# Kernel tuning notes

Hardware: AMD Instinct MI355X
Metric: run time of the kernel (lower is better)

The kernel has to match this reference:

```python
import jax, jax.numpy as jnp
import numpy as np
from math import sqrt

RELATIVE_CUTOFF = 128
VALUE_DIM = 64


def _skew(m):
    # m: (b, h, S, 2S-1) -> (b, h, S, S), out[i, j] = m[i, j - i + S - 1]
    b, h, S, _ = m.shape
    m = jnp.pad(m, ((0, 0), (0, 0), (0, 0), (0, 1)))          # (b,h,S,2S)
    m = m.reshape(b, h, 2 * S * S)
    m = jnp.pad(m, ((0, 0), (0, 0), (0, S - 1)))
    m = m.reshape(b, h, S + 1, 2 * S - 1)
    return m[:, :, :S, S - 1:]


def setup_inputs() -> dict:
    key = jax.random.key(0)
    ks = jax.random.split(key, 5)
    B, S, E, H, Dk, Dv = 2, 2048, 512, 8, 64, 64
    return {
        "xs": jax.random.normal(ks[0], (B, S, E), dtype=jnp.float32),
        "w_q": jax.random.normal(ks[1], (H, E, Dk), dtype=jnp.float32) * (1.0 / sqrt(E)),
        "w_k": jax.random.normal(ks[2], (H, E, Dk), dtype=jnp.float32) * (1.0 / sqrt(E)),
        "w_v": jax.random.normal(ks[3], (H, E, Dv), dtype=jnp.float32) * (1.0 / sqrt(E)),
        "w_o": jnp.ones((H,), dtype=jnp.float32),
        "a_k": jax.random.normal(ks[4], (2 * RELATIVE_CUTOFF + 1, Dk), dtype=jnp.float32) * 0.1,
    }


def reference(xs, w_q, w_k, w_v, w_o, a_k):
    S = xs.shape[1]
    queries = jnp.einsum("bse,heq->bhsq", xs, w_q)
    keys = jnp.einsum("bse,hek->bhsk", xs, w_k)
    values = jnp.einsum("bse,hev->bhsv", xs, w_v)

    # relative positional embeddings: pos in [-S+1, S-1], clamped to cutoff
    pos = jnp.clip(jnp.arange(-S + 1, S), -RELATIVE_CUTOFF, RELATIVE_CUTOFF) + RELATIVE_CUTOFF
    rel = a_k[pos]                                             # (2S-1, Dk)

    q_k = jnp.einsum("bhiq,bhjq->bhij", queries, keys)
    q_rel = _skew(jnp.einsum("bhiq,rq->bhir", queries, rel))   # (b,h,S,S)

    e = (q_k + q_rel) / sqrt(VALUE_DIM)
    alphas = jax.nn.softmax(e, axis=3)
    z = jnp.einsum("bhij,bhjv->bhiv", alphas, values)
    return jnp.einsum("bhsv,h->bsv", z, w_o)
```

## Files before the change

### kernel.cpp

```cpp
#include <hip/hip_runtime.h>
#include <hip/hip_bf16.h>

#define S_LEN 2048
#define E_DIM 512
#define D_DIM 64
#define H_NUM 8
#define B_NUM 2
#define BH_NUM 16
#define NQA 257
#define QAE_W 512
#define KSPLIT 2
#define NP 8
#define QTILE 256
#define BNDW 176

typedef _Float16 half8 __attribute__((ext_vector_type(8)));
typedef float f32x16 __attribute__((ext_vector_type(16)));
typedef unsigned int uint2v __attribute__((ext_vector_type(2)));
typedef unsigned int uint4v __attribute__((ext_vector_type(4)));

static __device__ __forceinline__ f32x16 MFMA(half8 a, half8 b, f32x16 c) {
    return __builtin_amdgcn_mfma_f32_32x32x16_f16(a, b, c, 0, 0, 0);
}
static __device__ __forceinline__ f32x16 ZERO16() {
    f32x16 z;
    #pragma unroll
    for (int i = 0; i < 16; ++i) z[i] = 0.f;
    return z;
}
static __device__ __forceinline__ unsigned int PKRTZ(float a, float b) {
    return __builtin_bit_cast(unsigned int, __builtin_amdgcn_cvt_pkrtz(a, b));
}

__global__ __launch_bounds__(256) void cast_x_kernel(
    const float* __restrict__ xs, _Float16* __restrict__ Xh)
{
    const int idx = (blockIdx.x * 256 + threadIdx.x) * 8;
    float4 a = *(const float4*)&xs[idx];
    float4 b = *(const float4*)&xs[idx + 4];
    half8 o;
    o[0] = (_Float16)a.x; o[1] = (_Float16)a.y; o[2] = (_Float16)a.z; o[3] = (_Float16)a.w;
    o[4] = (_Float16)b.x; o[5] = (_Float16)b.y; o[6] = (_Float16)b.z; o[7] = (_Float16)b.w;
    *(half8*)&Xh[idx] = o;
}

__global__ __launch_bounds__(256) void cast_wak_kernel(
    const float* __restrict__ w_q, const float* __restrict__ w_k,
    const float* __restrict__ w_v, const float* __restrict__ w_o,
    const float* __restrict__ a_k,
    _Float16* __restrict__ Wht, _Float16* __restrict__ akh)
{
    __shared__ float T[64][68];
    const int type = blockIdx.z;
    const int t = threadIdx.x;
    if (type == 3) {
        const int bn = blockIdx.y * 8 + blockIdx.x;
        if (bn >= 9) return;
        const int idx = (bn * 256 + t) * 8;
        if (idx < NQA * 64) {
            float4 a = *(const float4*)&a_k[idx];
            float4 b = *(const float4*)&a_k[idx + 4];
            half8 o;
            o[0] = (_Float16)a.x; o[1] = (_Float16)a.y; o[2] = (_Float16)a.z; o[3] = (_Float16)a.w;
            o[4] = (_Float16)b.x; o[5] = (_Float16)b.y; o[6] = (_Float16)b.z; o[7] = (_Float16)b.w;
            *(half8*)&akh[idx] = o;
        }
        return;
    }
    const int kt = blockIdx.x, h = blockIdx.y;
    const float* W = (type == 0) ? w_q : (type == 1) ? w_k : w_v;
    const float scale = (type == 0) ? 0.125f : (type == 2 ? w_o[h] : 1.0f);
    const int kr = t >> 2, nseg = (t & 3) * 16;
    #pragma unroll
    for (int i = 0; i < 4; ++i)
        *(float4*)&T[kr][nseg + 4 * i] =
            *(const float4*)&W[((size_t)h * 512 + kt * 64 + kr) * 64 + nseg + 4 * i];
    __syncthreads();
    const int nr = t >> 2, kseg = (t & 3) * 16;
    _Float16* dst = Wht + ((size_t)(type * 8 + h) * 64 + nr) * 512 + kt * 64 + kseg;
    #pragma unroll
    for (int i = 0; i < 2; ++i) {
        half8 o;
        #pragma unroll
        for (int j = 0; j < 8; ++j) o[j] = (_Float16)(T[kseg + 8 * i + j][nr] * scale);
        *(half8*)&dst[8 * i] = o;
    }
}

__global__ __launch_bounds__(256) void proj_mfma_kernel(
    const _Float16* __restrict__ Xh, const _Float16* __restrict__ Wht,
    const _Float16* __restrict__ akh,
    _Float16* __restrict__ Qh, _Float16* __restrict__ Kh,
    _Float16* __restrict__ Vt, _Float16* __restrict__ QAe)
{
    __shared__ __align__(16) _Float16 raw[30208];
    _Float16 (*Xlds)[128][72] = (_Float16(*)[128][72])raw;
    _Float16 (*Wlds)[64][72]  = (_Float16(*)[64][72])(raw + 18432);
    _Float16* ob  = raw;
    _Float16 (*ak)[72] = (_Float16(*)[72])(raw + 9216);
    _Float16* SLo = raw + 29952;
    _Float16* SHi = raw + 30080;

    const int mt = blockIdx.x, bh = blockIdx.y, type = blockIdx.z;
    const int b = bh >> 3, h = bh & 7;
    const int m0 = mt * 128;
    const int t = threadIdx.x, wid = t >> 6, lane = t & 63;
    const int lq = lane & 31, lh = lane >> 5;

    const _Float16* W = Wht + (size_t)(type * 8 + h) * 64 * 512;
    const _Float16* X = Xh + ((size_t)b * S_LEN + m0) * 512;

    const int xrow = t >> 1, xseg = (t & 1) * 32;
    const int wrow = t >> 2, wseg = (t & 3) * 16;

    #pragma unroll
    for (int i = 0; i < 4; ++i)
        *(half8*)&Xlds[0][xrow][xseg + 8 * i] =
            *(const half8*)&X[(size_t)xrow * 512 + xseg + 8 * i];
    #pragma unroll
    for (int i = 0; i < 2; ++i)
        *(half8*)&Wlds[0][wrow][wseg + 8 * i] =
            *(const half8*)&W[(size_t)wrow * 512 + wseg + 8 * i];
    __syncthreads();

    f32x16 acc[2];
    acc[0] = ZERO16(); acc[1] = ZERO16();
    int cur = 0;
    for (int c = 0; c < 8; ++c) {
        half8 xst[4], wst[2];
        if (c < 7) {
            const int k0 = (c + 1) * 64;
            #pragma unroll
            for (int i = 0; i < 4; ++i)
                xst[i] = *(const half8*)&X[(size_t)xrow * 512 + k0 + xseg + 8 * i];
            #pragma unroll
            for (int i = 0; i < 2; ++i)
                wst[i] = *(const half8*)&W[(size_t)wrow * 512 + k0 + wseg + 8 * i];
        }
        #pragma unroll
        for (int kc = 0; kc < 4; ++kc) {
            half8 a  = *(const half8*)&Xlds[cur][wid * 32 + lq][kc * 16 + lh * 8];
            half8 b0 = *(const half8*)&Wlds[cur][lq][kc * 16 + lh * 8];
            half8 b1 = *(const half8*)&Wlds[cur][32 + lq][kc * 16 + lh * 8];
            acc[0] = MFMA(a, b0, acc[0]);
            acc[1] = MFMA(a, b1, acc[1]);
        }
        if (c < 7) {
            #pragma unroll
            for (int i = 0; i < 4; ++i)
                *(half8*)&Xlds[cur ^ 1][xrow][xseg + 8 * i] = xst[i];
            #pragma unroll
            for (int i = 0; i < 2; ++i)
                *(half8*)&Wlds[cur ^ 1][wrow][wseg + 8 * i] = wst[i];
        }
        __syncthreads();
        cur ^= 1;
    }

    #pragma unroll
    for (int n = 0; n < 2; ++n)
        #pragma unroll
        for (int r = 0; r < 16; ++r) {
            int row = wid * 32 + (r & 3) + ((r >> 2) << 3) + (lh << 2);
            ob[row * 72 + n * 32 + lq] = (_Float16)acc[n][r];
        }
    __syncthreads();

    if (type == 2) {
        const int v = t >> 2, sseg = (t & 3) * 32;
        _Float16* dst = Vt + ((size_t)bh * 64 + v) * S_LEN + m0 + sseg;
        #pragma unroll
        for (int i = 0; i < 4; ++i) {
            half8 o;
            #pragma unroll
            for (int j = 0; j < 8; ++j) o[j] = ob[(sseg + 8 * i + j) * 72 + v];
            *(half8*)&dst[8 * i] = o;
        }
        return;
    }

    {
        _Float16* P = (type == 0) ? Qh : Kh;
        const int row = t >> 1, seg = (t & 1) * 32;
        _Float16* dst = P + ((size_t)bh * S_LEN + m0 + row) * 64 + seg;
        #pragma unroll
        for (int i = 0; i < 4; ++i)
            *(half8*)&dst[8 * i] = *(const half8*)&ob[row * 72 + seg + 8 * i];
    }
    if (type != 0) return;

    for (int r = t; r < 288; r += 256) {
        if (r < NQA) {
            #pragma unroll
            for (int i = 0; i < 8; ++i)
                *(half8*)&ak[r][8 * i] = *(const half8*)&akh[(size_t)r * 64 + 8 * i];
        } else {
            half8 z = {};
            #pragma unroll
            for (int i = 0; i < 8; ++i) *(half8*)&ak[r][8 * i] = z;
        }
    }
    __syncthreads();

    half8 qfr[4];
    #pragma unroll
    for (int kc = 0; kc < 4; ++kc)
        qfr[kc] = *(const half8*)&ob[(wid * 32 + lq) * 72 + kc * 16 + lh * 8];

    for (int nsub = 0; nsub < 9; ++nsub) {
        f32x16 qa = ZERO16();
        #pragma unroll
        for (int kc = 0; kc < 4; ++kc) {
            half8 bf = *(const half8*)&ak[nsub * 32 + lq][kc * 16 + lh * 8];
            qa = MFMA(qfr[kc], bf, qa);
        }
        const int col = nsub * 32 + lq;
        if (col < NQA) {
            #pragma unroll
            for (int r = 0; r < 16; ++r) {
                const int row = m0 + wid * 32 + (r & 3) + ((r >> 2) << 3) + (lh << 2);
                const _Float16 v = (_Float16)qa[r];
                QAe[((size_t)bh * S_LEN + row) * QAE_W + col + 128] = v;
                if (col == 0)   SLo[row - m0] = v;
                if (col == 256) SHi[row - m0] = v;
            }
        }
    }
    __syncthreads();

    const int prow = t >> 1, pseg = (t & 1) * 64;
    const _Float16 lo = SLo[prow], hi = SHi[prow];
    half8 vlo, vhi;
    #pragma unroll
    for (int j = 0; j < 8; ++j) { vlo[j] = lo; vhi[j] = hi; }
    _Float16* pb = QAe + ((size_t)bh * S_LEN + m0 + prow) * QAE_W;
    #pragma unroll
    for (int i = 0; i < 8; ++i) {
        *(half8*)&pb[pseg + 8 * i] = vlo;
        *(half8*)&pb[384 + pseg + 8 * i] = vhi;
    }
}

__global__ __launch_bounds__(512) void attn_kernel(
    const _Float16* __restrict__ Qh, const _Float16* __restrict__ Kh,
    const _Float16* __restrict__ Vt, const _Float16* __restrict__ QAe,
    _Float16* __restrict__ Po, float2* __restrict__ Ml)
{
    __shared__ __align__(16) char smraw[36864];
    _Float16 (*Klds)[64][72] = (_Float16(*)[64][72])smraw;
    _Float16 (*Vlds)[64][72] = (_Float16(*)[64][72])(smraw + 18432);
    _Float16* Obuf = (_Float16*)smraw;
    __shared__ __align__(16) _Float16 Bnd[8][32][BNDW];

    const int p0 = blockIdx.x;
    const int nb = (p0 & 7) * 32 + (p0 >> 3);
    const int bh = nb >> 4;
    const int rem = nb & 15;
    const int qt = rem & 7, ks = rem >> 3;
    const int i0 = qt * QTILE;
    const int kv0 = ks * 128;

    const int t = threadIdx.x, wid = t >> 6, lane = t & 63;
    const int lq = lane & 31, lh = lane >> 5;
    const int i0w = i0 + wid * 32;
    const int qg = i0w + lq;

    half8 qf[4];
    #pragma unroll
    for (int kc = 0; kc < 4; ++kc)
        qf[kc] = *(const half8*)&Qh[((size_t)bh * S_LEN + qg) * 64 + kc * 16 + lh * 8];

    const _Float16* qaeRow = QAe + ((size_t)bh * S_LEN + qg) * QAE_W;
    const float qa_lo = (float)qaeRow[128];
    const float qa_hi = (float)qaeRow[384];
    const _Float16* BndSrc = QAe + ((size_t)bh * S_LEN + i0w) * QAE_W;

    float rm = -1e30f, rl = 0.f;
    f32x16 acco[2];
    acco[0] = ZERO16(); acco[1] = ZERO16();

    const int srow = t >> 3, sseg = (t & 7) * 8;
    const _Float16* Kbase = Kh + (size_t)bh * S_LEN * 64;
    const _Float16* Vbase = Vt + ((size_t)bh * 64 + srow) * S_LEN;

    const int brow = lane >> 1;
    const int bhalf = (lane & 1) * 88;

    half8 kA, kB, vA, vB, breg[11];
    {
        const int js = kv0;
        *(half8*)&Klds[0][srow][sseg] = *(const half8*)&Kbase[(size_t)(js + srow) * 64 + sseg];
        *(half8*)&Klds[1][srow][sseg] = *(const half8*)&Kbase[(size_t)(js + 64 + srow) * 64 + sseg];
        *(half8*)&Vlds[0][srow][sseg] = *(const half8*)&Vbase[js + sseg];
        *(half8*)&Vlds[1][srow][sseg] = *(const half8*)&Vbase[js + 64 + sseg];
        const int j1 = 256 + kv0;
        kA = *(const half8*)&Kbase[(size_t)(j1 + srow) * 64 + sseg];
        kB = *(const half8*)&Kbase[(size_t)(j1 + 64 + srow) * 64 + sseg];
        vA = *(const half8*)&Vbase[j1 + sseg];
        vB = *(const half8*)&Vbase[j1 + 64 + sseg];
    }
    bool bA_n, bB_n; int cw0_n = 0;
    {
        const int d = kv0 - i0w;
        bA_n = (d > -191) && (d < 159);
        bB_n = (d > -255) && (d < 95);
        if (bA_n || bB_n) {
            const int dFB = bA_n ? d : d + 64;
            cw0_n = (dFB + 225) & ~7;
            cw0_n = cw0_n > 336 ? 336 : cw0_n;
            #pragma unroll
            for (int i = 0; i < 11; ++i)
                breg[i] = *(const half8*)&BndSrc[(size_t)brow * QAE_W + cw0_n + bhalf + i * 8];
        }
    }
    __syncthreads();

    for (int p = 0; p < NP; ++p) {
        const int diff = p * 256 + kv0 - i0w;
        const bool bA = bA_n, bB = bB_n;
        const int cw0 = cw0_n;

        if (bA || bB) {
            #pragma unroll
            for (int i = 0; i < 11; ++i)
                *(half8*)&Bnd[wid][brow][bhalf + i * 8] = breg[i];
        }

        f32x16 accs[4];
        accs[0] = ZERO16(); accs[1] = ZERO16(); accs[2] = ZERO16(); accs[3] = ZERO16();
        __builtin_amdgcn_s_setprio(1);
        #pragma unroll
        for (int kc = 0; kc < 4; ++kc) {
            half8 a0 = *(const half8*)&Klds[0][lq][kc * 16 + lh * 8];
            half8 a1 = *(const half8*)&Klds[0][32 + lq][kc * 16 + lh * 8];
            half8 b0 = *(const half8*)&Klds[1][lq][kc * 16 + lh * 8];
            half8 b1 = *(const half8*)&Klds[1][32 + lq][kc * 16 + lh * 8];
            accs[0] = MFMA(a0, qf[kc], accs[0]);
            accs[1] = MFMA(a1, qf[kc], accs[1]);
            accs[2] = MFMA(b0, qf[kc], accs[2]);
            accs[3] = MFMA(b1, qf[kc], accs[3]);
        }
        __builtin_amdgcn_s_setprio(0);

        float bunif = 0.f;
        if (diff >= 159) {
            bunif = qa_hi;
        } else if (diff <= -255) {
            bunif = qa_lo;
        } else {
            asm volatile("s_waitcnt lgkmcnt(0)" ::: "memory");
            __builtin_amdgcn_sched_barrier(0);
            const int pbA = diff + 256 - cw0 - lq;
            const int pbB = pbA + 64;
            if (bA) {
                #pragma unroll
                for (int m = 0; m < 2; ++m)
                    #pragma unroll
                    for (int r = 0; r < 16; ++r) {
                        const int keyoff = m * 32 + (r & 3) + ((r >> 2) << 3) + (lh << 2);
                        accs[m][r] += (float)Bnd[wid][lq][pbA + keyoff];
                    }
            } else {
                #pragma unroll
                for (int m = 0; m < 2; ++m)
                    #pragma unroll
                    for (int r = 0; r < 16; ++r) accs[m][r] += qa_lo;
            }
            if (bB) {
                #pragma unroll
                for (int m = 0; m < 2; ++m)
                    #pragma unroll
                    for (int r = 0; r < 16; ++r) {
                        const int keyoff = m * 32 + (r & 3) + ((r >> 2) << 3) + (lh << 2);
                        accs[2 + m][r] += (float)Bnd[wid][lq][pbB + keyoff];
                    }
            } else {
                #pragma unroll
                for (int m = 0; m < 2; ++m)
                    #pragma unroll
                    for (int r = 0; r < 16; ++r) accs[2 + m][r] += qa_hi;
            }
        }

        float t8[8];
        #pragma unroll
        for (int i = 0; i < 8; ++i)
            t8[i] = fmaxf(fmaxf(accs[0][i], accs[0][i + 8]),
                          fmaxf(accs[1][i], accs[1][i + 8]));
        #pragma unroll
        for (int i = 0; i < 8; ++i)
            t8[i] = fmaxf(t8[i], fmaxf(fmaxf(accs[2][i], accs[2][i + 8]),
                                       fmaxf(accs[3][i], accs[3][i + 8])));
        float tmax = fmaxf(fmaxf(fmaxf(t8[0], t8[1]), fmaxf(t8[2], t8[3])),
                           fmaxf(fmaxf(t8[4], t8[5]), fmaxf(t8[6], t8[7])));
        tmax = fmaxf(tmax, __shfl_xor(tmax, 32));
        const float mnew = fmaxf(rm, tmax + bunif);
        const bool resc = __any(mnew > rm);
        const float corr = __expf(rm - mnew);
        const float shift = mnew - bunif;
        rm = mnew;

        #pragma unroll
        for (int s = 0; s < 4; ++s)
            #pragma unroll
            for (int r = 0; r < 16; ++r)
                accs[s][r] = __expf(accs[s][r] - shift);

        float s8[8];
        #pragma unroll
        for (int i = 0; i < 8; ++i)
            s8[i] = ((accs[0][i] + accs[0][i + 8]) + (accs[1][i] + accs[1][i + 8]))
                  + ((accs[2][i] + accs[2][i + 8]) + (accs[3][i] + accs[3][i + 8]));
        float psum = ((s8[0] + s8[1]) + (s8[2] + s8[3])) +
                     ((s8[4] + s8[5]) + (s8[6] + s8[7]));
        psum += __shfl_xor(psum, 32);

        if (resc) {
            rl = rl * corr + psum;
            #pragma unroll
            for (int n = 0; n < 2; ++n)
                #pragma unroll
                for (int r = 0; r < 16; ++r) acco[n][r] *= corr;
        } else {
            rl += psum;
        }

        half8 pfA[4], pfB[4];
        #pragma unroll
        for (int kc = 0; kc < 4; ++kc) {
            {
                const int m = kc >> 1, rb = (kc & 1) * 8;
                unsigned int a01 = PKRTZ(accs[m][rb + 0], accs[m][rb + 1]);
                unsigned int a45 = PKRTZ(accs[m][rb + 4], accs[m][rb + 5]);
                unsigned int a23 = PKRTZ(accs[m][rb + 2], accs[m][rb + 3]);
                unsigned int a67 = PKRTZ(accs[m][rb + 6], accs[m][rb + 7]);
                uint2v r02 = __builtin_amdgcn_permlane32_swap(a01, a45, false, false);
                uint2v r13 = __builtin_amdgcn_permlane32_swap(a23, a67, false, false);
                uint4v wv;
                wv[0] = r02[0]; wv[1] = r13[0]; wv[2] = r02[1]; wv[3] = r13[1];
                pfA[kc] = __builtin_bit_cast(half8, wv);
            }
            {
                const int m = 2 + (kc >> 1), rb = (kc & 1) * 8;
                unsigned int a01 = PKRTZ(accs[m][rb + 0], accs[m][rb + 1]);
                unsigned int a45 = PKRTZ(accs[m][rb + 4], accs[m][rb + 5]);
                unsigned int a23 = PKRTZ(accs[m][rb + 2], accs[m][rb + 3]);
                unsigned int a67 = PKRTZ(accs[m][rb + 6], accs[m][rb + 7]);
                uint2v r02 = __builtin_amdgcn_permlane32_swap(a01, a45, false, false);
                uint2v r13 = __builtin_amdgcn_permlane32_swap(a23, a67, false, false);
                uint4v wv;
                wv[0] = r02[0]; wv[1] = r13[0]; wv[2] = r02[1]; wv[3] = r13[1];
                pfB[kc] = __builtin_bit_cast(half8, wv);
            }
        }

        __builtin_amdgcn_s_setprio(1);
        #pragma unroll
        for (int kc = 0; kc < 4; ++kc) {
            half8 v0 = *(const half8*)&Vlds[0][lq][kc * 16 + lh * 8];
            half8 v1 = *(const half8*)&Vlds[0][32 + lq][kc * 16 + lh * 8];
            acco[0] = MFMA(v0, pfA[kc], acco[0]);
            acco[1] = MFMA(v1, pfA[kc], acco[1]);
        }
        #pragma unroll
        for (int kc = 0; kc < 4; ++kc) {
            half8 v0 = *(const half8*)&Vlds[1][lq][kc * 16 + lh * 8];
            half8 v1 = *(const half8*)&Vlds[1][32 + lq][kc * 16 + lh * 8];
            acco[0] = MFMA(v0, pfB[kc], acco[0]);
            acco[1] = MFMA(v1, pfB[kc], acco[1]);
        }
        __builtin_amdgcn_s_setprio(0);

        {
            const int dn = diff + 256;
            bA_n = (p + 1 < NP) && (dn > -191) && (dn < 159);
            bB_n = (p + 1 < NP) && (dn > -255) && (dn < 95);
            if (bA_n || bB_n) {
                const int dFB = bA_n ? dn : dn + 64;
                cw0_n = (dFB + 225) & ~7;
                cw0_n = cw0_n > 336 ? 336 : cw0_n;
                #pragma unroll
                for (int i = 0; i < 11; ++i)
                    breg[i] = *(const half8*)&BndSrc[(size_t)brow * QAE_W + cw0_n + bhalf + i * 8];
            }
        }

        if (p + 1 < NP) {
            __syncthreads();
            *(half8*)&Klds[0][srow][sseg] = kA;
            *(half8*)&Klds[1][srow][sseg] = kB;
            *(half8*)&Vlds[0][srow][sseg] = vA;
            *(half8*)&Vlds[1][srow][sseg] = vB;
            if (p + 2 < NP) {
                const int jn = (p + 2) * 256 + kv0;
                kA = *(const half8*)&Kbase[(size_t)(jn + srow) * 64 + sseg];
                kB = *(const half8*)&Kbase[(size_t)(jn + 64 + srow) * 64 + sseg];
                vA = *(const half8*)&Vbase[jn + sseg];
                vB = *(const half8*)&Vbase[jn + 64 + sseg];
            }
            __syncthreads();
        }
    }

    __syncthreads();
    const int orow = wid * 32 + lq;
    #pragma unroll
    for (int n = 0; n < 2; ++n)
        #pragma unroll
        for (int rq = 0; rq < 4; ++rq) {
            uint2v hv;
            hv[0] = PKRTZ(acco[n][rq * 4 + 0], acco[n][rq * 4 + 1]);
            hv[1] = PKRTZ(acco[n][rq * 4 + 2], acco[n][rq * 4 + 3]);
            *(uint2v*)&Obuf[(size_t)orow * 72 + n * 32 + rq * 8 + lh * 4] = hv;
        }
    if (lh == 0)
        Ml[((size_t)ks * BH_NUM + bh) * S_LEN + qg] = make_float2(rm, rl);
    asm volatile("s_waitcnt lgkmcnt(0)" ::: "memory");
    __builtin_amdgcn_sched_barrier(0);
    const int rrow = wid * 32 + (lane >> 1);
    const int rseg = (lane & 1) * 32;
    _Float16* dst = Po + (((size_t)ks * BH_NUM + bh) * S_LEN + i0 + rrow) * 64 + rseg;
    #pragma unroll
    for (int i = 0; i < 4; ++i)
        *(half8*)&dst[8 * i] = *(const half8*)&Obuf[(size_t)rrow * 72 + rseg + 8 * i];
}

__global__ __launch_bounds__(256) void merge_kernel(
    const _Float16* __restrict__ Po, const float2* __restrict__ Ml,
    float* __restrict__ out)
{
    const int b = blockIdx.y;
    const int s = blockIdx.x * 32 + (threadIdx.x >> 3);
    const int v0 = (threadIdx.x & 7) * 8;
    float acc[8] = {0, 0, 0, 0, 0, 0, 0, 0};
    #pragma unroll
    for (int h = 0; h < 8; ++h) {
        const int bh = b * 8 + h;
        float m[KSPLIT], l[KSPLIT];
        #pragma unroll
        for (int p = 0; p < KSPLIT; ++p) {
            const float2 v = Ml[((size_t)p * BH_NUM + bh) * S_LEN + s];
            m[p] = v.x; l[p] = v.y;
        }
        float M = fmaxf(m[0], m[1]);
        float L = 0.f, w[KSPLIT];
        #pragma unroll
        for (int p = 0; p < KSPLIT; ++p) { w[p] = __expf(m[p] - M); L += w[p] * l[p]; }
        const float invL = 1.0f / L;
        #pragma unroll
        for (int p = 0; p < KSPLIT; ++p) {
            half8 o = *(const half8*)&Po[(((size_t)p * BH_NUM + bh) * S_LEN + s) * 64 + v0];
            const float wp = w[p] * invL;
            #pragma unroll
            for (int j = 0; j < 8; ++j) acc[j] += wp * (float)o[j];
        }
    }
    float4 o0 = {acc[0], acc[1], acc[2], acc[3]};
    float4 o1 = {acc[4], acc[5], acc[6], acc[7]};
    *(float4*)&out[((size_t)b * S_LEN + s) * 64 + v0] = o0;
    *(float4*)&out[((size_t)b * S_LEN + s) * 64 + v0 + 4] = o1;
}

extern "C" void kernel_launch(void* const* d_in, const int* in_sizes, int n_in,
                              void* d_out, int out_size, void* d_ws, size_t ws_size,
                              hipStream_t stream)
{
    const float* xs  = (const float*)d_in[0];
    const float* w_q = (const float*)d_in[1];
    const float* w_k = (const float*)d_in[2];
    const float* w_v = (const float*)d_in[3];
    const float* w_o = (const float*)d_in[4];
    const float* a_k = (const float*)d_in[5];
    float* out = (float*)d_out;

    char* w = (char*)d_ws;
    _Float16* Xh  = (_Float16*)w;  w += (size_t)B_NUM * S_LEN * E_DIM * 2;
    _Float16* Wht = (_Float16*)w;  w += (size_t)3 * H_NUM * 64 * 512 * 2;
    _Float16* akh = (_Float16*)w;  w += 33024;
    _Float16* Qh  = (_Float16*)w;  w += (size_t)BH_NUM * S_LEN * 64 * 2;
    _Float16* Kh  = (_Float16*)w;  w += (size_t)BH_NUM * S_LEN * 64 * 2;
    _Float16* Vt  = (_Float16*)w;  w += (size_t)BH_NUM * S_LEN * 64 * 2;
    _Float16* QAe = (_Float16*)w;  w += (size_t)BH_NUM * S_LEN * QAE_W * 2 + 1024;
    _Float16* Po  = (_Float16*)w;  w += (size_t)KSPLIT * BH_NUM * S_LEN * 64 * 2;
    float2*   Ml  = (float2*)w;

    cast_x_kernel<<<1024, 256, 0, stream>>>(xs, Xh);
    cast_wak_kernel<<<dim3(8, 8, 4), 256, 0, stream>>>(w_q, w_k, w_v, w_o, a_k, Wht, akh);
    proj_mfma_kernel<<<dim3(16, 16, 3), 256, 0, stream>>>(Xh, Wht, akh, Qh, Kh, Vt, QAe);
    attn_kernel<<<256, 512, 0, stream>>>(Qh, Kh, Vt, QAe, Po, Ml);
    merge_kernel<<<dim3(64, 2), 256, 0, stream>>>(Po, Ml, out);
}
```

Baseline: 79.69 us.

## Fuse x cast into projection and compute Q/K/V in one block

Removes the separate fp32-to-fp16 cast kernel for xs. The projection kernel now reads fp32 xs directly and converts it while staging into shared memory. Each block computes the Q, K and V projections together, sharing one X tile across three weight tiles, so X is loaded and converted once per tile rather than three times. The cost is a 3x smaller grid (256 blocks), more LDS (about 92KB) and more accumulator registers per thread, which lowers occupancy and serialises the three epilogues.

```diff
diff --git a/kernel.cpp b/kernel.cpp
--- a/kernel.cpp
+++ b/kernel.cpp
@@ -31,17 +31,11 @@
 static __device__ __forceinline__ unsigned int PKRTZ(float a, float b) {
     return __builtin_bit_cast(unsigned int, __builtin_amdgcn_cvt_pkrtz(a, b));
 }
-
-__global__ __launch_bounds__(256) void cast_x_kernel(
-    const float* __restrict__ xs, _Float16* __restrict__ Xh)
-{
-    const int idx = (blockIdx.x * 256 + threadIdx.x) * 8;
-    float4 a = *(const float4*)&xs[idx];
-    float4 b = *(const float4*)&xs[idx + 4];
-    half8 o;
-    o[0] = (_Float16)a.x; o[1] = (_Float16)a.y; o[2] = (_Float16)a.z; o[3] = (_Float16)a.w;
-    o[4] = (_Float16)b.x; o[5] = (_Float16)b.y; o[6] = (_Float16)b.z; o[7] = (_Float16)b.w;
-    *(half8*)&Xh[idx] = o;
+static __device__ __forceinline__ half8 CVT8(float4 a, float4 b) {
+    uint4v u;
+    u[0] = PKRTZ(a.x, a.y); u[1] = PKRTZ(a.z, a.w);
+    u[2] = PKRTZ(b.x, b.y); u[3] = PKRTZ(b.z, b.w);
+    return __builtin_bit_cast(half8, u);
 }
 
 __global__ __launch_bounds__(256) void cast_wak_kernel(
@@ -60,10 +54,7 @@
         if (idx < NQA * 64) {
             float4 a = *(const float4*)&a_k[idx];
             float4 b = *(const float4*)&a_k[idx + 4];
-            half8 o;
-            o[0] = (_Float16)a.x; o[1] = (_Float16)a.y; o[2] = (_Float16)a.z; o[3] = (_Float16)a.w;
-            o[4] = (_Float16)b.x; o[5] = (_Float16)b.y; o[6] = (_Float16)b.z; o[7] = (_Float16)b.w;
-            *(half8*)&akh[idx] = o;
+            *(half8*)&akh[idx] = CVT8(a, b);
         }
         return;
     }
@@ -87,107 +78,100 @@
     }
 }
 
-__global__ __launch_bounds__(256) void proj_mfma_kernel(
-    const _Float16* __restrict__ Xh, const _Float16* __restrict__ Wht,
+__global__ __launch_bounds__(256) void proj_qkv_kernel(
+    const float* __restrict__ xs, const _Float16* __restrict__ Wht,
     const _Float16* __restrict__ akh,
     _Float16* __restrict__ Qh, _Float16* __restrict__ Kh,
     _Float16* __restrict__ Vt, _Float16* __restrict__ QAe)
 {
-    __shared__ __align__(16) _Float16 raw[30208];
-    _Float16 (*Xlds)[128][72] = (_Float16(*)[128][72])raw;
-    _Float16 (*Wlds)[64][72]  = (_Float16(*)[64][72])(raw + 18432);
-    _Float16* ob  = raw;
-    _Float16 (*ak)[72] = (_Float16(*)[72])(raw + 9216);
-    _Float16* SLo = raw + 29952;
-    _Float16* SHi = raw + 30080;
-
-    const int mt = blockIdx.x, bh = blockIdx.y, type = blockIdx.z;
+    __shared__ __align__(16) _Float16 raw[46080];
+    _Float16 (*Xlds)[128][72]    = (_Float16(*)[128][72])raw;
+    _Float16 (*Wlds)[3][64][72]  = (_Float16(*)[3][64][72])(raw + 18432);
+    _Float16* ob = raw;
+    _Float16 (*ak)[72] = (_Float16(*)[72])(raw + 18432);
+    __shared__ _Float16 SLo[128], SHi[128];
+
+    const int mt = blockIdx.x, bh = blockIdx.y;
     const int b = bh >> 3, h = bh & 7;
     const int m0 = mt * 128;
     const int t = threadIdx.x, wid = t >> 6, lane = t & 63;
     const int lq = lane & 31, lh = lane >> 5;
 
-    const _Float16* W = Wht + (size_t)(type * 8 + h) * 64 * 512;
-    const _Float16* X = Xh + ((size_t)b * S_LEN + m0) * 512;
+    const float* X = xs + ((size_t)b * S_LEN + m0) * 512;
+    const _Float16* W0 = Wht + (size_t)(0 * 8 + h) * 64 * 512;
+    const _Float16* W1 = Wht + (size_t)(1 * 8 + h) * 64 * 512;
+    const _Float16* W2 = Wht + (size_t)(2 * 8 + h) * 64 * 512;
 
     const int xrow = t >> 1, xseg = (t & 1) * 32;
     const int wrow = t >> 2, wseg = (t & 3) * 16;
 
     #pragma unroll
-    for (int i = 0; i < 4; ++i)
-        *(half8*)&Xlds[0][xrow][xseg + 8 * i] =
-            *(const half8*)&X[(size_t)xrow * 512 + xseg + 8 * i];
-    #pragma unroll
-    for (int i = 0; i < 2; ++i)
-        *(half8*)&Wlds[0][wrow][wseg + 8 * i] =
-            *(const half8*)&W[(size_t)wrow * 512 + wseg + 8 * i];
+    for (int i = 0; i < 4; ++i) {
+        float4 a = *(const float4*)&X[(size_t)xrow * 512 + xseg + 8 * i];
+        float4 c = *(const float4*)&X[(size_t)xrow * 512 + xseg + 8 * i + 4];
+        *(half8*)&Xlds[0][xrow][xseg + 8 * i] = CVT8(a, c);
+    }
+    #pragma unroll
+    for (int i = 0; i < 2; ++i) {
+        *(half8*)&Wlds[0][0][wrow][wseg + 8 * i] = *(const half8*)&W0[(size_t)wrow * 512 + wseg + 8 * i];
+        *(half8*)&Wlds[0][1][wrow][wseg + 8 * i] = *(const half8*)&W1[(size_t)wrow * 512 + wseg + 8 * i];
+        *(half8*)&Wlds[0][2][wrow][wseg + 8 * i] = *(const half8*)&W2[(size_t)wrow * 512 + wseg + 8 * i];
+    }
     __syncthreads();
 
-    f32x16 acc[2];
-    acc[0] = ZERO16(); acc[1] = ZERO16();
+    f32x16 accQ[2], accK[2], accV[2];
+    accQ[0] = ZERO16(); accQ[1] = ZERO16();
+    accK[0] = ZERO16(); accK[1] = ZERO16();
+    accV[0] = ZERO16(); accV[1] = ZERO16();
+
     int cur = 0;
     for (int c = 0; c < 8; ++c) {
-        half8 xst[4], wst[2];
+        float4 xa[4], xb[4];
+        half8 w0a, w0b, w1a, w1b, w2a, w2b;
         if (c < 7) {
             const int k0 = (c + 1) * 64;
             #pragma unroll
+            for (int i = 0; i < 4; ++i) {
+                xa[i] = *(const float4*)&X[(size_t)xrow * 512 + k0 + xseg + 8 * i];
+                xb[i] = *(const float4*)&X[(size_t)xrow * 512 + k0 + xseg + 8 * i + 4];
+            }
+            w0a = *(const half8*)&W0[(size_t)wrow * 512 + k0 + wseg];
+            w0b = *(const half8*)&W0[(size_t)wrow * 512 + k0 + wseg + 8];
+            w1a = *(const half8*)&W1[(size_t)wrow * 512 + k0 + wseg];
+            w1b = *(const half8*)&W1[(size_t)wrow * 512 + k0 + wseg + 8];
+            w2a = *(const half8*)&W2[(size_t)wrow * 512 + k0 + wseg];
+            w2b = *(const half8*)&W2[(size_t)wrow * 512 + k0 + wseg + 8];
+        }
+        #pragma unroll
+        for (int kc = 0; kc < 4; ++kc) {
+            half8 a = *(const half8*)&Xlds[cur][wid * 32 + lq][kc * 16 + lh * 8];
+            half8 q0 = *(const half8*)&Wlds[cur][0][lq][kc * 16 + lh * 8];
+            half8 q1 = *(const half8*)&Wlds[cur][0][32 + lq][kc * 16 + lh * 8];
+            accQ[0] = MFMA(a, q0, accQ[0]);
+            accQ[1] = MFMA(a, q1, accQ[1]);
+            half8 k0f = *(const half8*)&Wlds[cur][1][lq][kc * 16 + lh * 8];
+            half8 k1f = *(const half8*)&Wlds[cur][1][32 + lq][kc * 16 + lh * 8];
+            accK[0] = MFMA(a, k0f, accK[0]);
+            accK[1] = MFMA(a, k1f, accK[1]);
+            half8 v0f = *(const half8*)&Wlds[cur][2][lq][kc * 16 + lh * 8];
+            half8 v1f = *(const half8*)&Wlds[cur][2][32 + lq][kc * 16 + lh * 8];
+            accV[0] = MFMA(a, v0f, accV[0]);
+            accV[1] = MFMA(a, v1f, accV[1]);
+        }
+        if (c < 7) {
+            #pragma unroll
             for (int i = 0; i < 4; ++i)
-                xst[i] = *(const half8*)&X[(size_t)xrow * 512 + k0 + xseg + 8 * i];
-            #pragma unroll
-            for (int i = 0; i < 2; ++i)
-                wst[i] = *(const half8*)&W[(size_t)wrow * 512 + k0 + wseg + 8 * i];
-        }
-        #pragma unroll
-        for (int kc = 0; kc < 4; ++kc) {
-            half8 a  = *(const half8*)&Xlds[cur][wid * 32 + lq][kc * 16 + lh * 8];
-            half8 b0 = *(const half8*)&Wlds[cur][lq][kc * 16 + lh * 8];
-            half8 b1 = *(const half8*)&Wlds[cur][32 + lq][kc * 16 + lh * 8];
-            acc[0] = MFMA(a, b0, acc[0]);
-            acc[1] = MFMA(a, b1, acc[1]);
-        }
-        if (c < 7) {
-            #pragma unroll
-            for (int i = 0; i < 4; ++i)
-                *(half8*)&Xlds[cur ^ 1][xrow][xseg + 8 * i] = xst[i];
-            #pragma unroll
-            for (int i = 0; i < 2; ++i)
-                *(half8*)&Wlds[cur ^ 1][wrow][wseg + 8 * i] = wst[i];
+                *(half8*)&Xlds[cur ^ 1][xrow][xseg + 8 * i] = CVT8(xa[i], xb[i]);
+            *(half8*)&Wlds[cur ^ 1][0][wrow][wseg]     = w0a;
+            *(half8*)&Wlds[cur ^ 1][0][wrow][wseg + 8] = w0b;
+            *(half8*)&Wlds[cur ^ 1][1][wrow][wseg]     = w1a;
+            *(half8*)&Wlds[cur ^ 1][1][wrow][wseg + 8] = w1b;
+            *(half8*)&Wlds[cur ^ 1][2][wrow][wseg]     = w2a;
+            *(half8*)&Wlds[cur ^ 1][2][wrow][wseg + 8] = w2b;
         }
         __syncthreads();
         cur ^= 1;
     }
-
-    #pragma unroll
-    for (int n = 0; n < 2; ++n)
-        #pragma unroll
-        for (int r = 0; r < 16; ++r) {
-            int row = wid * 32 + (r & 3) + ((r >> 2) << 3) + (lh << 2);
-            ob[row * 72 + n * 32 + lq] = (_Float16)acc[n][r];
-        }
-    __syncthreads();
-
-    if (type == 2) {
-        const int v = t >> 2, sseg = (t & 3) * 32;
-        _Float16* dst = Vt + ((size_t)bh * 64 + v) * S_LEN + m0 + sseg;
-        #pragma unroll
-        for (int i = 0; i < 4; ++i) {
-            half8 o;
-            #pragma unroll
-            for (int j = 0; j < 8; ++j) o[j] = ob[(sseg + 8 * i + j) * 72 + v];
-            *(half8*)&dst[8 * i] = o;
-        }
-        return;
-    }
-
-    {
-        _Float16* P = (type == 0) ? Qh : Kh;
-        const int row = t >> 1, seg = (t & 1) * 32;
-        _Float16* dst = P + ((size_t)bh * S_LEN + m0 + row) * 64 + seg;
-        #pragma unroll
-        for (int i = 0; i < 4; ++i)
-            *(half8*)&dst[8 * i] = *(const half8*)&ob[row * 72 + seg + 8 * i];
-    }
-    if (type != 0) return;
 
     for (int r = t; r < 288; r += 256) {
         if (r < NQA) {
@@ -200,12 +184,45 @@
             for (int i = 0; i < 8; ++i) *(half8*)&ak[r][8 * i] = z;
         }
     }
-    __syncthreads();
 
     half8 qfr[4];
-    #pragma unroll
-    for (int kc = 0; kc < 4; ++kc)
-        qfr[kc] = *(const half8*)&ob[(wid * 32 + lq) * 72 + kc * 16 + lh * 8];
+
+    #pragma unroll
+    for (int type = 0; type < 3; ++type) {
+        const f32x16* acc = (type == 0) ? accQ : (type == 1) ? accK : accV;
+        __syncthreads();
+        #pragma unroll
+        for (int n = 0; n < 2; ++n)
+            #pragma unroll
+            for (int r = 0; r < 16; ++r) {
+                int row = wid * 32 + (r & 3) + ((r >> 2) << 3) + (lh << 2);
+                ob[row * 72 + n * 32 + lq] = (_Float16)acc[n][r];
+            }
+        __syncthreads();
+        if (type == 0) {
+            #pragma unroll
+            for (int kc = 0; kc < 4; ++kc)
+                qfr[kc] = *(const half8*)&ob[(wid * 32 + lq) * 72 + kc * 16 + lh * 8];
+        }
+        if (type == 2) {
+            const int v = t >> 2, sseg = (t & 3) * 32;
+            _Float16* dst = Vt + ((size_t)bh * 64 + v) * S_LEN + m0 + sseg;
+            #pragma unroll
+            for (int i = 0; i < 4; ++i) {
+                half8 o;
+                #pragma unroll
+                for (int j = 0; j < 8; ++j) o[j] = ob[(sseg + 8 * i + j) * 72 + v];
+                *(half8*)&dst[8 * i] = o;
+            }
+        } else {
+            _Float16* P = (type == 0) ? Qh : Kh;
+            const int row = t >> 1, seg = (t & 1) * 32;
+            _Float16* dst = P + ((size_t)bh * S_LEN + m0 + row) * 64 + seg;
+            #pragma unroll
+            for (int i = 0; i < 4; ++i)
+                *(half8*)&dst[8 * i] = *(const half8*)&ob[row * 72 + seg + 8 * i];
+        }
+    }
 
     for (int nsub = 0; nsub < 9; ++nsub) {
         f32x16 qa = ZERO16();
@@ -574,7 +591,6 @@
     float* out = (float*)d_out;
 
     char* w = (char*)d_ws;
-    _Float16* Xh  = (_Float16*)w;  w += (size_t)B_NUM * S_LEN * E_DIM * 2;
     _Float16* Wht = (_Float16*)w;  w += (size_t)3 * H_NUM * 64 * 512 * 2;
     _Float16* akh = (_Float16*)w;  w += 33024;
     _Float16* Qh  = (_Float16*)w;  w += (size_t)BH_NUM * S_LEN * 64 * 2;
@@ -584,9 +600,8 @@
     _Float16* Po  = (_Float16*)w;  w += (size_t)KSPLIT * BH_NUM * S_LEN * 64 * 2;
     float2*   Ml  = (float2*)w;
 
-    cast_x_kernel<<<1024, 256, 0, stream>>>(xs, Xh);
     cast_wak_kernel<<<dim3(8, 8, 4), 256, 0, stream>>>(w_q, w_k, w_v, w_o, a_k, Wht, akh);
-    proj_mfma_kernel<<<dim3(16, 16, 3), 256, 0, stream>>>(Xh, Wht, akh, Qh, Kh, Vt, QAe);
+    proj_qkv_kernel<<<dim3(16, 16), 256, 0, stream>>>(xs, Wht, akh, Qh, Kh, Vt, QAe);
     attn_kernel<<<256, 512, 0, stream>>>(Qh, Kh, Vt, QAe, Po, Ml);
     merge_kernel<<<dim3(64, 2), 256, 0, stream>>>(Po, Ml, out);
 }
```

New measurement: 84.91 us. 1.07x slower.
